# Kernel tuning notes

Measured on AMD Instinct MI355X. Metric: run time of the kernel, lower is better.

## Reference

```python
import jax, jax.numpy as jnp
import numpy as np

SIGMA = 8.0
C_SIZE = 512
STRIDE = 8
BG_RATIO = 0.15
EPS = 1e-5


def setup_inputs() -> dict:
    key = jax.random.key(0)
    k1, k2 = jax.random.split(key)
    B, N = 16, 512
    # head-point coordinates uniformly in the crop [0, C_SIZE)
    points = jax.random.uniform(k1, (B, N, 2), dtype=jnp.float32) * C_SIZE
    # per-image shortest side sizes, realistic crop scales
    st_sizes = jax.random.uniform(k2, (B,), dtype=jnp.float32) * 256.0 + 256.0
    return {"points": points, "st_sizes": st_sizes}


def reference(points, st_sizes):
    # pixel-center coordinates of the downsampled density grid, [C]
    cood = jnp.arange(0, C_SIZE, STRIDE, dtype=jnp.float32) + STRIDE / 2.0
    B, N, _ = points.shape
    C = cood.shape[0]
    x = points[..., 0]  # [B, N]
    y = points[..., 1]  # [B, N]
    # (x - c)^2 == -2*x*c + x^2 + c^2 (the matmul trick in the original)
    x_dis = (x[..., None] - cood) ** 2  # [B, N, C]
    y_dis = (y[..., None] - cood) ** 2  # [B, N, C]
    # dis[b, p, i, j] = (y_p - cood_i)^2 + (x_p - cood_j)^2
    dis = y_dis[:, :, :, None] + x_dis[:, :, None, :]  # [B, N, C, C]
    dis = dis.reshape(B, N, C * C)  # [B, N, M]
    # background distance: per-pixel min over points, clamped at 0
    min_dis = jnp.clip(jnp.min(dis, axis=1, keepdims=True), 0.0)  # [B, 1, M]
    bg_dis = (st_sizes[:, None, None] * BG_RATIO) ** 2 / (min_dis + EPS)
    dis = jnp.concatenate([dis, bg_dis], axis=1)  # [B, N+1, M]
    logits = -dis / (2.0 * SIGMA ** 2)
    # softmax over the point (+background) axis, per pixel
    return jax.nn.softmax(logits, axis=1)
```

## Files before the change

kernel.cpp:

```cpp
#include <hip/hip_runtime.h>
#include <hip/hip_bf16.h>
#include <cstddef>

constexpr int NPT  = 512;
constexpr int C    = 64;
constexpr int M    = C * C;
constexpr int NP1  = NPT + 1;
constexpr float SIG2INV = 1.0f / 128.0f;
constexpr float BG_RATIO = 0.15f;
constexpr float EPS = 1e-5f;

__global__ __launch_bounds__(256) void pp_kernel(
    const float* __restrict__ points,
    const float* __restrict__ st,
    float* __restrict__ out)
{
    const int b = blockIdx.x >> 6;
    const int i = blockIdx.x & 63;
    const int t = threadIdx.x;
    const int j = t & 63;
    const int pc = t >> 6;

    const float cy = (float)(i * 8 + 4);
    const float cx = (float)(j * 8 + 4);

    __shared__ float2 pts[NPT];
    __shared__ float  red[256];
    __shared__ float  qs[C];
    __shared__ float  bgs[C];
    __shared__ float  rs[C];

    const float2* pb = (const float2*)(points + (size_t)b * NPT * 2);
    for (int p = t; p < NPT; p += 256) pts[p] = pb[p];
    __syncthreads();

    const int p0 = pc * 128, p1 = p0 + 128;

    float mind = 3.4e38f;
    #pragma unroll 8
    for (int p = p0; p < p1; ++p) {
        float2 xy = pts[p];
        float dy = xy.y - cy;
        float dx = xy.x - cx;
        float d  = fmaf(dx, dx, dy * dy);
        mind = fminf(mind, d);
    }
    red[t] = mind;
    __syncthreads();

    if (t < C) {
        float m0 = fminf(fminf(red[j], red[64 + j]),
                         fminf(red[128 + j], red[192 + j]));
        float s  = st[b] * BG_RATIO;
        float bg = (s * s) / (m0 + EPS);
        qs[j]  = fminf(m0, bg);
        bgs[j] = bg;
    }
    __syncthreads();

    const float q  = qs[j];
    const float qk = q * SIG2INV;

    float sum = 0.0f;
    #pragma unroll 8
    for (int p = p0; p < p1; ++p) {
        float2 xy = pts[p];
        float dy = xy.y - cy;
        float dx = xy.x - cx;
        float d  = fmaf(dx, dx, dy * dy);
        sum += __expf(fmaf(-d, SIG2INV, qk));
    }
    red[t] = sum;
    __syncthreads();

    if (t < C) {
        float s = (red[j] + red[64 + j]) + (red[128 + j] + red[192 + j]);
        s += __expf(fmaf(-bgs[j], SIG2INV, qs[j] * SIG2INV));
        rs[j] = 1.0f / s;
    }
    __syncthreads();

    const float r = rs[j];
    float* ob = out + (size_t)b * NP1 * M + (size_t)i * C + j;

    #pragma unroll 4
    for (int p = p0; p < p1; ++p) {
        float2 xy = pts[p];
        float dy = xy.y - cy;
        float dx = xy.x - cx;
        float d  = fmaf(dx, dx, dy * dy);
        ob[(size_t)p * M] = __expf(fmaf(-d, SIG2INV, qk)) * r;
    }
    if (t < C) {
        ob[(size_t)NPT * M] = __expf(fmaf(-bgs[j], SIG2INV, qk)) * r;
    }
}

extern "C" void kernel_launch(void* const* d_in, const int* in_sizes, int n_in,
                              void* d_out, int out_size, void* d_ws, size_t ws_size,
                              hipStream_t stream) {
    const float* points = (const float*)d_in[0];
    const float* st     = (const float*)d_in[1];
    float* out          = (float*)d_out;

    const int B = in_sizes[1];
    dim3 grid(B * C);
    dim3 block(256);
    pp_kernel<<<grid, block, 0, stream>>>(points, st, out);
}
```

Baseline: 147.6 us.

## Fuse min and sum passes, compute four pixels per thread with vector stores

Merges the min-distance pass and the exp-sum pass into one loop by dropping the max-shift in the softmax. Each thread now handles four adjacent pixels over 32 points. Partial results are combined with wave shuffles plus one shared-memory step, and outputs are written as float4. This removes one full pass of distance and exp work and one barrier, and widens the global stores. In exchange, the softmax no longer subtracts its stabilising term, so it can underflow if every point is far from a pixel.

```diff
diff --git a/kernel.cpp b/kernel.cpp
--- a/kernel.cpp
+++ b/kernel.cpp
@@ -2,11 +2,11 @@
 #include <hip/hip_bf16.h>
 #include <cstddef>
 
-constexpr int NPT  = 512;
-constexpr int C    = 64;
-constexpr int M    = C * C;
-constexpr int NP1  = NPT + 1;
-constexpr float SIG2INV = 1.0f / 128.0f;
+constexpr int NPT = 512;
+constexpr int C   = 64;
+constexpr int M   = C * C;
+constexpr int NP1 = NPT + 1;
+constexpr float K = 1.0f / 128.0f;
 constexpr float BG_RATIO = 0.15f;
 constexpr float EPS = 1e-5f;
 
@@ -15,84 +15,97 @@
     const float* __restrict__ st,
     float* __restrict__ out)
 {
-    const int b = blockIdx.x >> 6;
-    const int i = blockIdx.x & 63;
-    const int t = threadIdx.x;
-    const int j = t & 63;
-    const int pc = t >> 6;
+    const int b    = blockIdx.x >> 6;
+    const int i    = blockIdx.x & 63;
+    const int t    = threadIdx.x;
+    const int lane = t & 63;
+    const int w    = t >> 6;
+    const int jg   = t & 15;
+    const int pc   = t >> 4;
 
-    const float cy = (float)(i * 8 + 4);
-    const float cx = (float)(j * 8 + 4);
+    const float cy  = (float)(i * 8 + 4);
+    const float cx0 = (float)(jg * 32 + 4);
+    const float cx1 = cx0 + 8.0f;
+    const float cx2 = cx0 + 16.0f;
+    const float cx3 = cx0 + 24.0f;
 
     __shared__ float2 pts[NPT];
-    __shared__ float  red[256];
-    __shared__ float  qs[C];
+    __shared__ float4 redmin[4][16];
+    __shared__ float4 redsum[4][16];
+    __shared__ float  rs[C];
     __shared__ float  bgs[C];
-    __shared__ float  rs[C];
 
     const float2* pb = (const float2*)(points + (size_t)b * NPT * 2);
     for (int p = t; p < NPT; p += 256) pts[p] = pb[p];
     __syncthreads();
 
-    const int p0 = pc * 128, p1 = p0 + 128;
+    const int p0 = pc * 32;
 
-    float mind = 3.4e38f;
-    #pragma unroll 8
-    for (int p = p0; p < p1; ++p) {
-        float2 xy = pts[p];
-        float dy = xy.y - cy;
-        float dx = xy.x - cx;
-        float d  = fmaf(dx, dx, dy * dy);
-        mind = fminf(mind, d);
+    float4 mn = make_float4(3.4e38f, 3.4e38f, 3.4e38f, 3.4e38f);
+    float4 sm = make_float4(0.f, 0.f, 0.f, 0.f);
+    #pragma unroll 4
+    for (int k = 0; k < 32; ++k) {
+        float2 xy = pts[p0 + k];
+        float dy  = xy.y - cy;
+        float dy2 = dy * dy;
+        float dx0 = xy.x - cx0, dx1 = xy.x - cx1, dx2 = xy.x - cx2, dx3 = xy.x - cx3;
+        float d0 = fmaf(dx0, dx0, dy2);
+        float d1 = fmaf(dx1, dx1, dy2);
+        float d2 = fmaf(dx2, dx2, dy2);
+        float d3 = fmaf(dx3, dx3, dy2);
+        mn.x = fminf(mn.x, d0); mn.y = fminf(mn.y, d1);
+        mn.z = fminf(mn.z, d2); mn.w = fminf(mn.w, d3);
+        sm.x += __expf(-d0 * K); sm.y += __expf(-d1 * K);
+        sm.z += __expf(-d2 * K); sm.w += __expf(-d3 * K);
     }
-    red[t] = mind;
+
+    #pragma unroll
+    for (int off = 16; off <= 32; off <<= 1) {
+        mn.x = fminf(mn.x, __shfl_xor(mn.x, off));
+        mn.y = fminf(mn.y, __shfl_xor(mn.y, off));
+        mn.z = fminf(mn.z, __shfl_xor(mn.z, off));
+        mn.w = fminf(mn.w, __shfl_xor(mn.w, off));
+        sm.x += __shfl_xor(sm.x, off);
+        sm.y += __shfl_xor(sm.y, off);
+        sm.z += __shfl_xor(sm.z, off);
+        sm.w += __shfl_xor(sm.w, off);
+    }
+    if (lane < 16) { redmin[w][lane] = mn; redsum[w][lane] = sm; }
     __syncthreads();
 
     if (t < C) {
-        float m0 = fminf(fminf(red[j], red[64 + j]),
-                         fminf(red[128 + j], red[192 + j]));
-        float s  = st[b] * BG_RATIO;
-        float bg = (s * s) / (m0 + EPS);
-        qs[j]  = fminf(m0, bg);
-        bgs[j] = bg;
+        const float* rm = (const float*)redmin;
+        const float* rq = (const float*)redsum;
+        float m0 = fminf(fminf(rm[t], rm[64 + t]), fminf(rm[128 + t], rm[192 + t]));
+        float s0 = (rq[t] + rq[64 + t]) + (rq[128 + t] + rq[192 + t]);
+        float ss = st[b] * BG_RATIO;
+        float bg = (ss * ss) / (m0 + EPS);
+        float tot = s0 + __expf(-bg * K);
+        bgs[t] = bg;
+        rs[t]  = 1.0f / tot;
     }
     __syncthreads();
 
-    const float q  = qs[j];
-    const float qk = q * SIG2INV;
+    const float4 r4 = *(const float4*)&rs[jg * 4];
 
-    float sum = 0.0f;
-    #pragma unroll 8
-    for (int p = p0; p < p1; ++p) {
-        float2 xy = pts[p];
-        float dy = xy.y - cy;
-        float dx = xy.x - cx;
-        float d  = fmaf(dx, dx, dy * dy);
-        sum += __expf(fmaf(-d, SIG2INV, qk));
+    float* ob = out + (size_t)b * NP1 * M + (size_t)p0 * M + i * C + jg * 4;
+    #pragma unroll 4
+    for (int k = 0; k < 32; ++k) {
+        float2 xy = pts[p0 + k];
+        float dy  = xy.y - cy;
+        float dy2 = dy * dy;
+        float dx0 = xy.x - cx0, dx1 = xy.x - cx1, dx2 = xy.x - cx2, dx3 = xy.x - cx3;
+        float4 v;
+        v.x = __expf(-fmaf(dx0, dx0, dy2) * K) * r4.x;
+        v.y = __expf(-fmaf(dx1, dx1, dy2) * K) * r4.y;
+        v.z = __expf(-fmaf(dx2, dx2, dy2) * K) * r4.z;
+        v.w = __expf(-fmaf(dx3, dx3, dy2) * K) * r4.w;
+        *(float4*)(ob + (size_t)k * M) = v;
     }
-    red[t] = sum;
-    __syncthreads();
 
     if (t < C) {
-        float s = (red[j] + red[64 + j]) + (red[128 + j] + red[192 + j]);
-        s += __expf(fmaf(-bgs[j], SIG2INV, qs[j] * SIG2INV));
-        rs[j] = 1.0f / s;
-    }
-    __syncthreads();
-
-    const float r = rs[j];
-    float* ob = out + (size_t)b * NP1 * M + (size_t)i * C + j;
-
-    #pragma unroll 4
-    for (int p = p0; p < p1; ++p) {
-        float2 xy = pts[p];
-        float dy = xy.y - cy;
-        float dx = xy.x - cx;
-        float d  = fmaf(dx, dx, dy * dy);
-        ob[(size_t)p * M] = __expf(fmaf(-d, SIG2INV, qk)) * r;
-    }
-    if (t < C) {
-        ob[(size_t)NPT * M] = __expf(fmaf(-bgs[j], SIG2INV, qk)) * r;
+        out[(size_t)b * NP1 * M + (size_t)NPT * M + i * C + t] =
+            __expf(-bgs[t] * K) * rs[t];
     }
 }
 
```

Result: faster. 141.1 us (-4.4%).
